# Optimization experiments

Hardware: AMD Instinct MI355X
Metric: run time of the kernel (lower is better)

Reference implementation:

```python
import jax, jax.numpy as jnp
import numpy as np

D = 1024          # model_dim
BD = D // 2       # bottleneck_dim
K = 64            # num_splats
B, S = 8, 2048


def setup_inputs() -> dict:
    key = jax.random.key(0)
    ks = jax.random.split(key, 12)
    sc = 0.02
    return {
        "token_embeddings": jax.random.normal(ks[0], (B, S, D), jnp.float32),
        "splat_influences": jax.random.uniform(ks[1], (B, S, K), jnp.float32),
        # encoder: Linear(D -> BD), stored [in, out]
        "enc_W": jax.random.normal(ks[2], (D, BD), jnp.float32) * sc,
        "enc_b": jnp.zeros((BD,), jnp.float32),
        # per-splat transforms: K x Linear(BD -> BD)
        "trans_W": jax.random.normal(ks[3], (K, BD, BD), jnp.float32) * sc,
        "trans_b": jnp.zeros((K, BD), jnp.float32),
        # decoder: Linear(BD -> D)
        "dec_W": jax.random.normal(ks[4], (BD, D), jnp.float32) * sc,
        "dec_b": jnp.zeros((D,), jnp.float32),
        # flow gate: Linear(D -> D) + sigmoid
        "gate_W": jax.random.normal(ks[5], (D, D), jnp.float32) * sc,
        "gate_b": jnp.zeros((D,), jnp.float32),
    }


def reference(token_embeddings, splat_influences, enc_W, enc_b,
              trans_W, trans_b, dec_W, dec_b, gate_W, gate_b):
    # gather: [B,K,S] @ [B,S,D] -> [B,K,D]
    influences_t = jnp.swapaxes(splat_influences, 1, 2)          # [B,K,S]
    gathered = jnp.einsum('bks,bsd->bkd', influences_t, token_embeddings)
    total = jnp.clip(influences_t.sum(axis=2, keepdims=True), 1e-8, None)  # [B,K,1]
    gathered = gathered / total
    # encoder (dropout inactive at eval)
    encoded = jax.nn.relu(gathered @ enc_W + enc_b)              # [B,K,BD]
    # per-splat transform as grouped matmul
    transformed = jnp.einsum('bkd,kde->bke', encoded, trans_W) + trans_b  # [B,K,BD]
    decoded = transformed @ dec_W + dec_b                        # [B,K,D]
    # scatter back to tokens: [B,S,K] @ [B,K,D]
    flow = jnp.einsum('bsk,bkd->bsd', splat_influences, decoded)
    gate = jax.nn.sigmoid(token_embeddings @ gate_W + gate_b)    # [B,S,D]
    return flow * gate
```

## Files before the change

kernel.cpp:

```cpp
#include <hip/hip_runtime.h>

#define BB 8
#define SS 2048
#define DD 1024
#define BDD 512
#define NSP 64

typedef __attribute__((ext_vector_type(8))) short bf16x8;
typedef __attribute__((ext_vector_type(4))) float f32x4;
typedef unsigned short u16;
typedef unsigned int u32;

__device__ __forceinline__ u16 f2bf(float f) {
  u32 u = __builtin_bit_cast(u32, f);
  u = u + 0x7fffu + ((u >> 16) & 1u);
  return (u16)(u >> 16);
}

__device__ __forceinline__ void gl_lds16(const void* g, void* l) {
  __builtin_amdgcn_global_load_lds((const __attribute__((address_space(1))) void*)g,
                                   (__attribute__((address_space(3))) void*)l,
                                   16, 0, 0);
}

__global__ void k_prep(const float* __restrict__ tok, const float* __restrict__ infl,
                       const float* __restrict__ gw, u16* __restrict__ tokbf,
                       u16* __restrict__ tokT, u16* __restrict__ inflbf,
                       u16* __restrict__ inflT, float* __restrict__ rsum,
                       u16* __restrict__ gwt) {
  __shared__ __align__(16) char smraw[128 * 41 * 4];
  u16(*tile)[80] = (u16(*)[80])smraw;
  float(*ps)[64] = (float(*)[64])(smraw + 64 * 80 * 2);
  float(*gt)[33] = (float(*)[33])smraw;
  int bid = blockIdx.x;
  int t = threadIdx.x;

  if (bid < 2048) {
    u32* t32 = (u32*)smraw;
    int C0 = (bid & 15) * 64;
    int R0 = (bid >> 4) * 128;
    int b = R0 >> 11, s0 = R0 & 2047;
    int lc = (t & 7) * 8;
#pragma unroll
    for (int i = 0; i < 4; ++i) {
      int r = (t >> 3) + i * 32;
      const float* src = tok + (size_t)(R0 + r) * DD + C0 + lc;
      float4 a = *(const float4*)src;
      float4 bq = *(const float4*)(src + 4);
      uint4 v;
      v.x = f2bf(a.x) | ((u32)f2bf(a.y) << 16);
      v.y = f2bf(a.z) | ((u32)f2bf(a.w) << 16);
      v.z = f2bf(bq.x) | ((u32)f2bf(bq.y) << 16);
      v.w = f2bf(bq.z) | ((u32)f2bf(bq.w) << 16);
      *(uint4*)(tokbf + (size_t)(R0 + r) * DD + C0 + lc) = v;
      int cbase = r * 41 + (t & 7) * 4;
      t32[cbase + 0] = v.x;
      t32[cbase + 1] = v.y;
      t32[cbase + 2] = v.z;
      t32[cbase + 3] = v.w;
    }
    __syncthreads();
    int dp = t >> 3;
    int si = (t & 7) * 8;
    size_t tb = (size_t)b * DD * SS;
#pragma unroll
    for (int h = 0; h < 2; ++h) {
      int sseg = si + h * 64;
      u32 w[8];
#pragma unroll
      for (int j = 0; j < 8; ++j) w[j] = t32[(sseg + j) * 41 + dp];
      uint4 vlo, vhi;
      vlo.x = (w[0] & 0xffffu) | (w[1] << 16);
      vlo.y = (w[2] & 0xffffu) | (w[3] << 16);
      vlo.z = (w[4] & 0xffffu) | (w[5] << 16);
      vlo.w = (w[6] & 0xffffu) | (w[7] << 16);
      vhi.x = (w[0] >> 16) | (w[1] & 0xffff0000u);
      vhi.y = (w[2] >> 16) | (w[3] & 0xffff0000u);
      vhi.z = (w[4] >> 16) | (w[5] & 0xffff0000u);
      vhi.w = (w[6] >> 16) | (w[7] & 0xffff0000u);
      size_t pbase = tb + (size_t)((s0 >> 6) + h) * (DD * 64);
      *(uint4*)(tokT + pbase + (size_t)(C0 + 2 * dp) * 64 + si) = vlo;
      *(uint4*)(tokT + pbase + (size_t)(C0 + 2 * dp + 1) * 64 + si) = vhi;
    }
  } else if (bid < 2304) {
    int R0 = (bid - 2048) * 64;
    int b = R0 >> 11, s0 = R0 & 2047;
    int st = s0 >> 6;
    int lr = t >> 3, lc = (t & 7) * 8;
    float col[8];
#pragma unroll
    for (int j = 0; j < 8; ++j) col[j] = 0.f;
#pragma unroll
    for (int i = 0; i < 2; ++i) {
      int r = lr + i * 32;
      const float* src = infl + (size_t)(R0 + r) * NSP + lc;
      float4 a = *(const float4*)src;
      float4 bq = *(const float4*)(src + 4);
      col[0] += a.x; col[1] += a.y; col[2] += a.z; col[3] += a.w;
      col[4] += bq.x; col[5] += bq.y; col[6] += bq.z; col[7] += bq.w;
      uint4 v;
      v.x = f2bf(a.x) | ((u32)f2bf(a.y) << 16);
      v.y = f2bf(a.z) | ((u32)f2bf(a.w) << 16);
      v.z = f2bf(bq.x) | ((u32)f2bf(bq.y) << 16);
      v.w = f2bf(bq.z) | ((u32)f2bf(bq.w) << 16);
      *(uint4*)(inflbf + (size_t)(R0 + r) * NSP + lc) = v;
      *(uint4*)&tile[r][lc] = v;
    }
#pragma unroll
    for (int j = 0; j < 8; ++j) ps[lr][lc + j] = col[j];
    __syncthreads();
    if (t < 64) {
      float s = 0.f;
#pragma unroll
      for (int rr = 0; rr < 32; ++rr) s += ps[rr][t];
      rsum[((size_t)b * 32 + st) * 64 + t] = s;
    }
    int sseg = (t & 7) * 8;
    size_t ibase = (size_t)b * NSP * SS + (size_t)st * (NSP * 64);
#pragma unroll
    for (int i = 0; i < 2; ++i) {
      int dcol = (t >> 3) + i * 32;
      u16 a0 = tile[sseg + 0][dcol], a1 = tile[sseg + 1][dcol];
      u16 a2 = tile[sseg + 2][dcol], a3 = tile[sseg + 3][dcol];
      u16 a4 = tile[sseg + 4][dcol], a5 = tile[sseg + 5][dcol];
      u16 a6 = tile[sseg + 6][dcol], a7 = tile[sseg + 7][dcol];
      uint4 v;
      v.x = a0 | ((u32)a1 << 16);
      v.y = a2 | ((u32)a3 << 16);
      v.z = a4 | ((u32)a5 << 16);
      v.w = a6 | ((u32)a7 << 16);
      *(uint4*)(inflT + ibase + (size_t)dcol * 64 + sseg) = v;
    }
  } else {
    int g = bid - 2304;
    int n0 = (g & 31) * 32, k0 = (g >> 5) * 32;
    int tx = t & 31, ty = t >> 5;
#pragma unroll
    for (int r = 0; r < 4; ++r) {
      int kr = ty + r * 8;
      gt[kr][tx] = gw[(k0 + kr) * DD + n0 + tx];
    }
    __syncthreads();
#pragma unroll
    for (int r = 0; r < 4; ++r) {
      int nc = ty + r * 8;
      gwt[(n0 + nc) * DD + k0 + tx] = f2bf(gt[tx][nc]);
    }
  }
}

__global__ __launch_bounds__(256) void k_gather_mfma(const u16* __restrict__ inflT,
                                                     const u16* __restrict__ tokT,
                                                     float* __restrict__ pg) {
  __shared__ u16 As[64 * 64];
  __shared__ u16 Bs[64 * 64];
  int t = threadIdx.x;
  int l = t & 63, w = t >> 6;
  int wr = w >> 1, wc = w & 1;
  int n0 = blockIdx.x * 64;
  int b = blockIdx.y;
  int sq = blockIdx.z;
  int l15 = l & 15, lh = l >> 4;
  int srow = t >> 3, scol = (t & 7) * 8;

  const u16* ap = inflT + (size_t)b * NSP * SS;
  const u16* bp = tokT + (size_t)b * DD * SS;

  f32x4 acc[2][2];
#pragma unroll
  for (int i = 0; i < 2; ++i)
#pragma unroll
    for (int j = 0; j < 2; ++j) acc[i][j] = (f32x4){0.f, 0.f, 0.f, 0.f};

  for (int kt = 0; kt < 8; ++kt) {
    int pc = sq * 8 + kt;
    const u16* app = ap + (size_t)pc * (NSP * 64);
    const u16* bpp = bp + (size_t)pc * (DD * 64);
#pragma unroll
    for (int i = 0; i < 2; ++i) {
      int row = srow + i * 32;
      gl_lds16(app + row * 64 + scol, &As[row * 64 + scol]);
      gl_lds16(bpp + (n0 + row) * 64 + scol, &Bs[row * 64 + scol]);
    }
    __syncthreads();
#pragma unroll
    for (int ks = 0; ks < 2; ++ks) {
      bf16x8 af[2], bfv[2];
#pragma unroll
      for (int mi = 0; mi < 2; ++mi)
        af[mi] = *(const bf16x8*)&As[(wr * 32 + mi * 16 + l15) * 64 + ks * 32 + lh * 8];
#pragma unroll
      for (int ni = 0; ni < 2; ++ni)
        bfv[ni] = *(const bf16x8*)&Bs[(wc * 32 + ni * 16 + l15) * 64 + ks * 32 + lh * 8];
#pragma unroll
      for (int mi = 0; mi < 2; ++mi)
#pragma unroll
        for (int ni = 0; ni < 2; ++ni)
          acc[mi][ni] = __builtin_amdgcn_mfma_f32_16x16x32_bf16(af[mi], bfv[ni], acc[mi][ni], 0, 0, 0);
    }
    __syncthreads();
  }

#pragma unroll
  for (int mi = 0; mi < 2; ++mi)
#pragma unroll
    for (int ni = 0; ni < 2; ++ni)
#pragma unroll
      for (int r = 0; r < 4; ++r) {
        int krow = wr * 32 + mi * 16 + lh * 4 + r;
        int dcol = n0 + wc * 32 + ni * 16 + l15;
        pg[((size_t)sq * 512 + b * NSP + krow) * DD + dcol] = acc[mi][ni][r];
      }
}

__global__ void k_enc_part(const float* __restrict__ pg, const float* __restrict__ rsum,
                           const float* __restrict__ encW, float* __restrict__ pe) {
  __shared__ float gl[8][128];
  int dq = blockIdx.x, mt = blockIdx.y;
  int m0 = mt * 8, d0 = dq * 128;
  int t = threadIdx.x;
  {
    int r = t >> 5, c = t & 31;
    float s[4] = {0.f, 0.f, 0.f, 0.f};
#pragma unroll
    for (int q = 0; q < 4; ++q) {
      const float* qp = pg + ((size_t)q * 512 + m0 + r) * DD + d0;
      s[0] += qp[c]; s[1] += qp[c + 32]; s[2] += qp[c + 64]; s[3] += qp[c + 96];
    }
    int mrow = m0 + r;
    int bq = mrow >> 6, kq = mrow & 63;
    float tt = 0.f;
#pragma unroll
    for (int st = 0; st < 32; ++st) tt += rsum[((size_t)bq * 32 + st) * 64 + kq];
    float rt = 1.f / fmaxf(tt, 1e-8f);
    gl[r][c] = s[0] * rt;
    gl[r][c + 32] = s[1] * rt;
    gl[r][c + 64] = s[2] * rt;
    gl[r][c + 96] = s[3] * rt;
  }
  __syncthreads();
  int n4 = (t & 127) * 4, mh = (t >> 7) * 4;
  float4 acc[4];
#pragma unroll
  for (int m = 0; m < 4; ++m) acc[m] = (float4){0.f, 0.f, 0.f, 0.f};
  for (int i = 0; i < 128; ++i) {
    float4 wv = *(const float4*)(encW + (d0 + i) * BDD + n4);
#pragma unroll
    for (int m = 0; m < 4; ++m) {
      float g = gl[mh + m][i];
      acc[m].x += g * wv.x; acc[m].y += g * wv.y;
      acc[m].z += g * wv.z; acc[m].w += g * wv.w;
    }
  }
#pragma unroll
  for (int m = 0; m < 4; ++m)
    *(float4*)(pe + ((size_t)dq * 512 + m0 + mh + m) * BDD + n4) = acc[m];
}

__global__ void k_trans_part(const float* __restrict__ pe, const float* __restrict__ encB,
                             const float* __restrict__ trW, float* __restrict__ pt) {
  __shared__ float el[8][64];
  int dq = blockIdx.x, ks = blockIdx.y;
  int d0 = dq * 64;
  int t = threadIdx.x;
  {
    int r = t >> 5, c = t & 31;
    int m = r * NSP + ks;
    float s1 = 0.f, s2 = 0.f;
#pragma unroll
    for (int p = 0; p < 8; ++p) {
      const float* qp = pe + ((size_t)p * 512 + m) * BDD + d0;
      s1 += qp[c]; s2 += qp[c + 32];
    }
    el[r][c] = fmaxf(s1 + encB[d0 + c], 0.f);
    el[r][c + 32] = fmaxf(s2 + encB[d0 + c + 32], 0.f);
  }
  __syncthreads();
  int n4 = (t & 127) * 4, mh = (t >> 7) * 4;
  float4 acc[4];
#pragma unroll
  for (int m = 0; m < 4; ++m) acc[m] = (float4){0.f, 0.f, 0.f, 0.f};
  for (int i = 0; i < 64; ++i) {
    float4 wv = *(const float4*)(trW + ((size_t)ks * BDD + d0 + i) * BDD + n4);
#pragma unroll
    for (int m = 0; m < 4; ++m) {
      float g = el[mh + m][i];
      acc[m].x += g * wv.x; acc[m].y += g * wv.y;
      acc[m].z += g * wv.z; acc[m].w += g * wv.w;
    }
  }
#pragma unroll
  for (int m = 0; m < 4; ++m)
    *(float4*)(pt + ((size_t)dq * 512 + (mh + m) * NSP + ks) * BDD + n4) = acc[m];
}

__global__ void k_dec_part(const float* __restrict__ pt, const float* __restrict__ trB,
                           const float* __restrict__ decW, float* __restrict__ pd) {
  __shared__ float tl[8][64];
  int dq = blockIdx.x, mt = blockIdx.y;
  int m0 = mt * 8, d0 = dq * 64;
  int t = threadIdx.x;
  {
    int r = t >> 5, c = t & 31;
    int m = m0 + r;
    float s1 = 0.f, s2 = 0.f;
#pragma unroll
    for (int p = 0; p < 8; ++p) {
      const float* qp = pt + ((size_t)p * 512 + m) * BDD + d0;
      s1 += qp[c]; s2 += qp[c + 32];
    }
    tl[r][c] = s1 + trB[(m & 63) * BDD + d0 + c];
    tl[r][c + 32] = s2 + trB[(m & 63) * BDD + d0 + c + 32];
  }
  __syncthreads();
  int n4 = t * 4;
  float4 acc[8];
#pragma unroll
  for (int m = 0; m < 8; ++m) acc[m] = (float4){0.f, 0.f, 0.f, 0.f};
  for (int i = 0; i < 64; ++i) {
    float4 wv = *(const float4*)(decW + (d0 + i) * DD + n4);
#pragma unroll
    for (int m = 0; m < 8; ++m) {
      float g = tl[m][i];
      acc[m].x += g * wv.x; acc[m].y += g * wv.y;
      acc[m].z += g * wv.z; acc[m].w += g * wv.w;
    }
  }
#pragma unroll
  for (int m = 0; m < 8; ++m)
    *(float4*)(pd + ((size_t)dq * 512 + m0 + m) * DD + n4) = acc[m];
}

__global__ void red_dec(const float* __restrict__ pd, const float* __restrict__ decB,
                        u16* __restrict__ decT) {
  __shared__ u16 st[64][34];
  int nt = blockIdx.x, b = blockIdx.y;
  int n0 = nt * 32;
  int t = threadIdx.x;
  int nn = t & 31, kg = t >> 5;
  float db = decB[n0 + nn];
#pragma unroll
  for (int ki = 0; ki < 8; ++ki) {
    int ks = kg * 8 + ki;
    float s = db;
#pragma unroll
    for (int p = 0; p < 8; ++p)
      s += pd[((size_t)p * 512 + b * NSP + ks) * DD + n0 + nn];
    st[ks][nn] = f2bf(s);
  }
  __syncthreads();
  int nr = t >> 3, kseg = (t & 7) * 8;
  uint4 v;
  v.x = st[kseg + 0][nr] | ((u32)st[kseg + 1][nr] << 16);
  v.y = st[kseg + 2][nr] | ((u32)st[kseg + 3][nr] << 16);
  v.z = st[kseg + 4][nr] | ((u32)st[kseg + 5][nr] << 16);
  v.w = st[kseg + 6][nr] | ((u32)st[kseg + 7][nr] << 16);
  *(uint4*)(decT + ((size_t)b * DD + n0 + nr) * NSP + kseg) = v;
}


#define GVM(n) asm volatile("s_waitcnt vmcnt(" #n ")" ::: "memory");

#define GSTA(sl, k0, p)                                                        \
  { int e = (p)*512 + t; int row = e >> 3; int cs = ((e & 7) ^ (row & 7)) * 8; \
    gl_lds16(tokbf + (size_t)(m0 + row) * DD + (k0) + cs, &As[sl][e * 8]); }
#define GSTB(sl, k0, p)                                                        \
  { int e = (p)*512 + t; int row = e >> 3; int cs = ((e & 7) ^ (row & 7)) * 8; \
    gl_lds16(gwt + (size_t)(n0 + row) * DD + (k0) + cs, &Bs[sl][e * 8]); }
#define SAI(sl, p)                                                             \
  { int e = (p)*512 + t; int row = e >> 3; int cs = ((e & 7) ^ (row & 7)) * 8; \
    gl_lds16(inflbf + ((size_t)bb * SS + s0m + row) * NSP + cs, &As[sl][e * 8]); }
#define SBD(sl, p)                                                             \
  { int e = (p)*512 + t; int row = e >> 3; int cs = ((e & 7) ^ (row & 7)) * 8; \
    gl_lds16(decT + ((size_t)bb * DD + n0 + row) * NSP + cs, &Bs[sl][e * 8]); }

#define GLOADB(sl)                                                             \
  _Pragma("unroll")                                                            \
  for (int nf = 0; nf < 2; ++nf) {                                             \
    int br = wc * 32 + nf * 16 + l15;                                          \
    bfv[nf][0] = *(const bf16x8*)&Bs[sl][br * 64 + c0];                        \
    bfv[nf][1] = *(const bf16x8*)&Bs[sl][br * 64 + c1];                        \
  }

#define GPH(sl, mq, VMW, STG, LDB)                                             \
  {                                                                            \
    VMW                                                                        \
    __builtin_amdgcn_s_barrier();                                              \
    LDB                                                                        \
    bf16x8 af[4][2];                                                           \
    _Pragma("unroll")                                                          \
    for (int mf = 0; mf < 4; ++mf) {                                           \
      int ar = (mq)*64 + mf * 16 + l15;                                        \
      af[mf][0] = *(const bf16x8*)&As[sl][ar * 64 + c0];                       \
      af[mf][1] = *(const bf16x8*)&As[sl][ar * 64 + c1];                       \
    }                                                                          \
    STG                                                                        \
    __builtin_amdgcn_s_setprio(1);                                             \
    _Pragma("unroll")                                                          \
    for (int mf = 0; mf < 4; ++mf)                                             \
      _Pragma("unroll")                                                        \
      for (int nf = 0; nf < 2; ++nf) {                                         \
        acc[(mq)*4 + mf][nf] = __builtin_amdgcn_mfma_f32_16x16x32_bf16(af[mf][0], bfv[nf][0], acc[(mq)*4 + mf][nf], 0, 0, 0); \
        acc[(mq)*4 + mf][nf] = __builtin_amdgcn_mfma_f32_16x16x32_bf16(af[mf][1], bfv[nf][1], acc[(mq)*4 + mf][nf], 0, 0, 0); \
      }                                                                        \
    __builtin_amdgcn_s_setprio(0);                                             \
    __builtin_amdgcn_s_barrier();                                              \
  }

#define GT_FULL(sl, osl, k1)                                                   \
  {                                                                            \
    bf16x8 bfv[2][2];                                                          \
    GPH(sl, 0, GVM(3), GSTB(osl, k1, 0) GSTB(osl, k1, 1), GLOADB(sl))          \
    GPH(sl, 1, GVM(4), GSTB(osl, k1, 2) GSTB(osl, k1, 3), )                    \
    GPH(sl, 2, GVM(5), GSTA(osl, k1, 0) GSTA(osl, k1, 1), )                    \
    GPH(sl, 3, GVM(6), GSTA(osl, k1, 2) GSTA(osl, k1, 3), )                    \
  }
#define GT_LAST2(sl)                                                           \
  {                                                                            \
    bf16x8 bfv[2][2];                                                          \
    GPH(sl, 0, GVM(3), SAI(0, 0) SAI(0, 1), GLOADB(sl))                        \
    GPH(sl, 1, GVM(4), SAI(0, 2) SAI(0, 3), )                                  \
    GPH(sl, 2, GVM(5), SBD(0, 0) SBD(0, 1), )                                  \
    GPH(sl, 3, GVM(6), SBD(0, 2) SBD(0, 3), )                                  \
  }

__global__ __launch_bounds__(512, 1) void k_gate(const u16* __restrict__ tokbf,
                                                 const u16* __restrict__ gwt,
                                                 const u16* __restrict__ inflbf,
                                                 const u16* __restrict__ decT,
                                                 const float* __restrict__ gateB,
                                                 float* __restrict__ outp) {
  __shared__ u16 As[2][256 * 64];
  __shared__ u16 Bs[2][256 * 64];
  int t = threadIdx.x;
  int l = t & 63, wc = t >> 6;
  int bid = blockIdx.x;
  int wg = (bid & 7) * 32 + (bid >> 3);
  int mt = wg & 63, nt = wg >> 6;
  int m0 = mt * 256, n0 = nt * 256;
  int l15 = l & 15, lh = l >> 4;
  int x7 = l15 & 7;
  int c0 = (lh ^ x7) * 8;
  int c1 = ((4 + lh) ^ x7) * 8;
  int bb = m0 >> 11, s0m = m0 & 2047;

  f32x4 acc[16][2];
#pragma unroll
  for (int i = 0; i < 16; ++i)
#pragma unroll
    for (int j = 0; j < 2; ++j) acc[i][j] = (f32x4){0.f, 0.f, 0.f, 0.f};

  GSTB(0, 0, 0) GSTB(0, 0, 1) GSTB(0, 0, 2) GSTB(0, 0, 3)
  GSTA(0, 0, 0) GSTA(0, 0, 1) GSTA(0, 0, 2) GSTA(0, 0, 3)

#pragma unroll 1
  for (int i = 0; i < 7; ++i) {
    GT_FULL(0, 1, (2 * i + 1) * 64)
    GT_FULL(1, 0, (2 * i + 2) * 64)
  }
  GT_FULL(0, 1, 960)
  GT_LAST2(1)

  GVM(0)
  __builtin_amdgcn_s_barrier();

  {
    float gb[2];
#pragma unroll
    for (int nf = 0; nf < 2; ++nf) gb[nf] = gateB[n0 + wc * 32 + nf * 16 + l15];
    bf16x8 bfv[2][2];
    GLOADB(0)
#pragma unroll
    for (int mq = 0; mq < 4; ++mq) {
      bf16x8 af[4][2];
#pragma unroll
      for (int mf = 0; mf < 4; ++mf) {
        int ar = mq * 64 + mf * 16 + l15;
        af[mf][0] = *(const bf16x8*)&As[0][ar * 64 + c0];
        af[mf][1] = *(const bf16x8*)&As[0][ar * 64 + c1];
      }
      f32x4 accf[4][2];
#pragma unroll
      for (int mf = 0; mf < 4; ++mf)
#pragma unroll
        for (int nf = 0; nf < 2; ++nf) accf[mf][nf] = (f32x4){0.f, 0.f, 0.f, 0.f};
      __builtin_amdgcn_s_setprio(1);
#pragma unroll
      for (int mf = 0; mf < 4; ++mf)
#pragma unroll
        for (int nf = 0; nf < 2; ++nf) {
          accf[mf][nf] = __builtin_amdgcn_mfma_f32_16x16x32_bf16(af[mf][0], bfv[nf][0], accf[mf][nf], 0, 0, 0);
          accf[mf][nf] = __builtin_amdgcn_mfma_f32_16x16x32_bf16(af[mf][1], bfv[nf][1], accf[mf][nf], 0, 0, 0);
        }
      __builtin_amdgcn_s_setprio(0);
#pragma unroll
      for (int mf = 0; mf < 4; ++mf)
#pragma unroll
        for (int nf = 0; nf < 2; ++nf)
#pragma unroll
          for (int r = 0; r < 4; ++r) {
            int mr = m0 + (mq * 4 + mf) * 16 + lh * 4 + r;
            int nc = n0 + wc * 32 + nf * 16 + l15;
            float z = acc[mq * 4 + mf][nf][r] + gb[nf];
            float gate = 1.f / (1.f + __expf(-z));
            outp[(size_t)mr * DD + nc] = accf[mf][nf][r] * gate;
          }
    }
  }
}

extern "C" void kernel_launch(void* const* d_in, const int* in_sizes, int n_in,
                              void* d_out, int out_size, void* d_ws, size_t ws_size,
                              hipStream_t stream) {
  const float* tok = (const float*)d_in[0];
  const float* infl = (const float*)d_in[1];
  const float* encW = (const float*)d_in[2];
  const float* encB = (const float*)d_in[3];
  const float* trW = (const float*)d_in[4];
  const float* trB = (const float*)d_in[5];
  const float* decW = (const float*)d_in[6];
  const float* decB = (const float*)d_in[7];
  const float* gw = (const float*)d_in[8];
  const float* gateB = (const float*)d_in[9];
  float* outp = (float*)d_out;

  char* wsp = (char*)d_ws;
  u16* tokbf = (u16*)(wsp);
  u16* gwt = (u16*)(wsp + 33554432);
  u16* inflbf = (u16*)(wsp + 35651584);
  u16* decT = (u16*)(wsp + 41945088);
  u16* tokT = (u16*)(wsp + 42993664);
  float* pe = (float*)(wsp + 42993664);
  float* pt = (float*)(wsp + 42993664 + 8388608);
  u16* inflT = (u16*)(wsp + 76548096);
  float* rsum = (float*)(wsp + 78645248);
  float* scratch = (float*)(wsp + 78710784);

  k_prep<<<dim3(3328), dim3(256), 0, stream>>>(tok, infl, gw, tokbf, tokT, inflbf,
                                               inflT, rsum, gwt);
  k_gather_mfma<<<dim3(16, 8, 4), dim3(256), 0, stream>>>(inflT, tokT, scratch);
  k_enc_part<<<dim3(8, 64), dim3(256), 0, stream>>>(scratch, rsum, encW, pe);
  k_trans_part<<<dim3(8, 64), dim3(256), 0, stream>>>(pe, encB, trW, pt);
  k_dec_part<<<dim3(8, 64), dim3(256), 0, stream>>>(pt, trB, decW, scratch);
  red_dec<<<dim3(32, 8), dim3(256), 0, stream>>>(scratch, decB, decT);
  k_gate<<<dim3(256), dim3(512), 0, stream>>>(tokbf, gwt, inflbf, decT, gateB, outp);
}
```

Measured before the change: 158.5 us.

## Drop transposed token buffer; transpose tokens in LDS inside gather kernel

The prep kernel no longer writes a transposed bf16 copy of the token embeddings (32 MB of extra global writes). The gather kernel instead loads row-major bf16 tokens and scatters them transposed into shared memory with 16 scalar u16 stores per thread. This trades global write traffic and an LDS transpose in prep for strided, bank-conflict-prone 2-byte LDS stores in the gather loop.

```diff
diff --git a/kernel.cpp b/kernel.cpp
--- a/kernel.cpp
+++ b/kernel.cpp
@@ -25,65 +25,27 @@
 
 __global__ void k_prep(const float* __restrict__ tok, const float* __restrict__ infl,
                        const float* __restrict__ gw, u16* __restrict__ tokbf,
-                       u16* __restrict__ tokT, u16* __restrict__ inflbf,
-                       u16* __restrict__ inflT, float* __restrict__ rsum,
-                       u16* __restrict__ gwt) {
-  __shared__ __align__(16) char smraw[128 * 41 * 4];
+                       u16* __restrict__ inflbf, u16* __restrict__ inflT,
+                       float* __restrict__ rsum, u16* __restrict__ gwt) {
+  __shared__ __align__(16) char smraw[64 * 80 * 2 + 32 * 64 * 4];
   u16(*tile)[80] = (u16(*)[80])smraw;
   float(*ps)[64] = (float(*)[64])(smraw + 64 * 80 * 2);
   float(*gt)[33] = (float(*)[33])smraw;
   int bid = blockIdx.x;
   int t = threadIdx.x;
 
-  if (bid < 2048) {
-    u32* t32 = (u32*)smraw;
-    int C0 = (bid & 15) * 64;
-    int R0 = (bid >> 4) * 128;
-    int b = R0 >> 11, s0 = R0 & 2047;
-    int lc = (t & 7) * 8;
-#pragma unroll
-    for (int i = 0; i < 4; ++i) {
-      int r = (t >> 3) + i * 32;
-      const float* src = tok + (size_t)(R0 + r) * DD + C0 + lc;
-      float4 a = *(const float4*)src;
-      float4 bq = *(const float4*)(src + 4);
-      uint4 v;
-      v.x = f2bf(a.x) | ((u32)f2bf(a.y) << 16);
-      v.y = f2bf(a.z) | ((u32)f2bf(a.w) << 16);
-      v.z = f2bf(bq.x) | ((u32)f2bf(bq.y) << 16);
-      v.w = f2bf(bq.z) | ((u32)f2bf(bq.w) << 16);
-      *(uint4*)(tokbf + (size_t)(R0 + r) * DD + C0 + lc) = v;
-      int cbase = r * 41 + (t & 7) * 4;
-      t32[cbase + 0] = v.x;
-      t32[cbase + 1] = v.y;
-      t32[cbase + 2] = v.z;
-      t32[cbase + 3] = v.w;
-    }
-    __syncthreads();
-    int dp = t >> 3;
-    int si = (t & 7) * 8;
-    size_t tb = (size_t)b * DD * SS;
-#pragma unroll
-    for (int h = 0; h < 2; ++h) {
-      int sseg = si + h * 64;
-      u32 w[8];
-#pragma unroll
-      for (int j = 0; j < 8; ++j) w[j] = t32[(sseg + j) * 41 + dp];
-      uint4 vlo, vhi;
-      vlo.x = (w[0] & 0xffffu) | (w[1] << 16);
-      vlo.y = (w[2] & 0xffffu) | (w[3] << 16);
-      vlo.z = (w[4] & 0xffffu) | (w[5] << 16);
-      vlo.w = (w[6] & 0xffffu) | (w[7] << 16);
-      vhi.x = (w[0] >> 16) | (w[1] & 0xffff0000u);
-      vhi.y = (w[2] >> 16) | (w[3] & 0xffff0000u);
-      vhi.z = (w[4] >> 16) | (w[5] & 0xffff0000u);
-      vhi.w = (w[6] >> 16) | (w[7] & 0xffff0000u);
-      size_t pbase = tb + (size_t)((s0 >> 6) + h) * (DD * 64);
-      *(uint4*)(tokT + pbase + (size_t)(C0 + 2 * dp) * 64 + si) = vlo;
-      *(uint4*)(tokT + pbase + (size_t)(C0 + 2 * dp + 1) * 64 + si) = vhi;
-    }
-  } else if (bid < 2304) {
-    int R0 = (bid - 2048) * 64;
+  if (bid < 8192) {
+    size_t i = ((size_t)bid * 256 + t) * 8;
+    float4 a = *(const float4*)(tok + i);
+    float4 bq = *(const float4*)(tok + i + 4);
+    uint4 v;
+    v.x = f2bf(a.x) | ((u32)f2bf(a.y) << 16);
+    v.y = f2bf(a.z) | ((u32)f2bf(a.w) << 16);
+    v.z = f2bf(bq.x) | ((u32)f2bf(bq.y) << 16);
+    v.w = f2bf(bq.z) | ((u32)f2bf(bq.w) << 16);
+    *(uint4*)(tokbf + i) = v;
+  } else if (bid < 8448) {
+    int R0 = (bid - 8192) * 64;
     int b = R0 >> 11, s0 = R0 & 2047;
     int st = s0 >> 6;
     int lr = t >> 3, lc = (t & 7) * 8;
@@ -132,7 +94,7 @@
       *(uint4*)(inflT + ibase + (size_t)dcol * 64 + sseg) = v;
     }
   } else {
-    int g = bid - 2304;
+    int g = bid - 8448;
     int n0 = (g & 31) * 32, k0 = (g >> 5) * 32;
     int tx = t & 31, ty = t >> 5;
 #pragma unroll
@@ -150,7 +112,7 @@
 }
 
 __global__ __launch_bounds__(256) void k_gather_mfma(const u16* __restrict__ inflT,
-                                                     const u16* __restrict__ tokT,
+                                                     const u16* __restrict__ tokbf,
                                                      float* __restrict__ pg) {
   __shared__ u16 As[64 * 64];
   __shared__ u16 Bs[64 * 64];
@@ -164,7 +126,8 @@
   int srow = t >> 3, scol = (t & 7) * 8;
 
   const u16* ap = inflT + (size_t)b * NSP * SS;
-  const u16* bp = tokT + (size_t)b * DD * SS;
+  int s = t >> 2;
+  int dseg = (t & 3) * 16;
 
   f32x4 acc[2][2];
 #pragma unroll
@@ -175,12 +138,33 @@
   for (int kt = 0; kt < 8; ++kt) {
     int pc = sq * 8 + kt;
     const u16* app = ap + (size_t)pc * (NSP * 64);
-    const u16* bpp = bp + (size_t)pc * (DD * 64);
 #pragma unroll
     for (int i = 0; i < 2; ++i) {
       int row = srow + i * 32;
       gl_lds16(app + row * 64 + scol, &As[row * 64 + scol]);
-      gl_lds16(bpp + (n0 + row) * 64 + scol, &Bs[row * 64 + scol]);
+    }
+    {
+      const u16* src = tokbf + ((size_t)(b * SS + pc * 64 + s)) * DD + n0 + dseg;
+      uint4 q0 = *(const uint4*)src;
+      uint4 q1 = *(const uint4*)(src + 8);
+      u32 wd0 = q0.x, wd1 = q0.y, wd2 = q0.z, wd3 = q0.w;
+      u32 wd4 = q1.x, wd5 = q1.y, wd6 = q1.z, wd7 = q1.w;
+      Bs[(dseg + 0) * 64 + s] = (u16)wd0;
+      Bs[(dseg + 1) * 64 + s] = (u16)(wd0 >> 16);
+      Bs[(dseg + 2) * 64 + s] = (u16)wd1;
+      Bs[(dseg + 3) * 64 + s] = (u16)(wd1 >> 16);
+      Bs[(dseg + 4) * 64 + s] = (u16)wd2;
+      Bs[(dseg + 5) * 64 + s] = (u16)(wd2 >> 16);
+      Bs[(dseg + 6) * 64 + s] = (u16)wd3;
+      Bs[(dseg + 7) * 64 + s] = (u16)(wd3 >> 16);
+      Bs[(dseg + 8) * 64 + s] = (u16)wd4;
+      Bs[(dseg + 9) * 64 + s] = (u16)(wd4 >> 16);
+      Bs[(dseg + 10) * 64 + s] = (u16)wd5;
+      Bs[(dseg + 11) * 64 + s] = (u16)(wd5 >> 16);
+      Bs[(dseg + 12) * 64 + s] = (u16)wd6;
+      Bs[(dseg + 13) * 64 + s] = (u16)(wd6 >> 16);
+      Bs[(dseg + 14) * 64 + s] = (u16)wd7;
+      Bs[(dseg + 15) * 64 + s] = (u16)(wd7 >> 16);
     }
     __syncthreads();
 #pragma unroll
@@ -529,16 +513,15 @@
   u16* gwt = (u16*)(wsp + 33554432);
   u16* inflbf = (u16*)(wsp + 35651584);
   u16* decT = (u16*)(wsp + 41945088);
-  u16* tokT = (u16*)(wsp + 42993664);
   float* pe = (float*)(wsp + 42993664);
   float* pt = (float*)(wsp + 42993664 + 8388608);
   u16* inflT = (u16*)(wsp + 76548096);
   float* rsum = (float*)(wsp + 78645248);
   float* scratch = (float*)(wsp + 78710784);
 
-  k_prep<<<dim3(3328), dim3(256), 0, stream>>>(tok, infl, gw, tokbf, tokT, inflbf,
+  k_prep<<<dim3(9472), dim3(256), 0, stream>>>(tok, infl, gw, tokbf, inflbf,
                                                inflT, rsum, gwt);
-  k_gather_mfma<<<dim3(16, 8, 4), dim3(256), 0, stream>>>(inflT, tokT, scratch);
+  k_gather_mfma<<<dim3(16, 8, 4), dim3(256), 0, stream>>>(inflT, tokbf, scratch);
   k_enc_part<<<dim3(8, 64), dim3(256), 0, stream>>>(scratch, rsum, encW, pe);
   k_trans_part<<<dim3(8, 64), dim3(256), 0, stream>>>(pe, encB, trW, pt);
   k_dec_part<<<dim3(8, 64), dim3(256), 0, stream>>>(pt, trB, decW, scratch);
```

After: 150.3 us. -5.2%, faster.
